# Kernel optimization log

Hardware: AMD Instinct MI355X
Metric: run time of the kernel (lower is better)

The kernel has to match this reference:

```python
import jax, jax.numpy as jnp
import numpy as np

HEADS = 16
HEAD_DIM = 64

def setup_inputs() -> dict:
    key = jax.random.key(0)
    ks = jax.random.split(key, 5)
    S, B, H = 1024, 4, 1024
    scale = 1.0 / np.sqrt(H)
    return {
        "hidden_states": jax.random.normal(ks[0], (S, B, H), jnp.float32),
        "attention_mask": jnp.zeros((B * HEADS, 1, S), jnp.float32),
        "Wq": jax.random.normal(ks[1], (H, H), jnp.float32) * scale,
        "bq": jnp.zeros((H,), jnp.float32),
        "Wk": jax.random.normal(ks[2], (H, H), jnp.float32) * scale,
        "bk": jnp.zeros((H,), jnp.float32),
        "Wv": jax.random.normal(ks[3], (H, H), jnp.float32) * scale,
        "bv": jnp.zeros((H,), jnp.float32),
    }

def reference(hidden_states, attention_mask, Wq, bq, Wk, bk, Wv, bv):
    S, B, H = hidden_states.shape
    d = HEAD_DIM
    inv_sqrt_d = 1.0 / np.sqrt(d)
    # QKV projections (torch Linear: x @ W.T + b)
    q = hidden_states @ Wq.T + bq  # (S, B, H)
    k = hidden_states @ Wk.T + bk
    v = hidden_states @ Wv.T + bv
    # (S, B*heads, d) -> (B*heads, S, d)
    q = q.reshape(S, B * HEADS, d).transpose(1, 0, 2)
    k = k.reshape(S, B * HEADS, d).transpose(1, 0, 2)
    v = v.reshape(S, B * HEADS, d).transpose(1, 0, 2)
    # SDDMM: scaled scores + additive mask -> (B*heads, S, S)
    scores = jnp.einsum('nsd,ntd->nst', q, k) * inv_sqrt_d + attention_mask
    probs = jax.nn.softmax(scores, axis=-1)
    # AV bmm -> (B*heads, S, d); note: dropout in source is seeded but never applied
    ctx = jnp.einsum('nst,ntd->nsd', probs, v)
    # back to (S, B, hidden)
    ctx = ctx.transpose(1, 0, 2).reshape(S, B, H)
    return ctx
```

## Files before the change

kernel.cpp:

```cpp
#include <hip/hip_runtime.h>
#include <hip/hip_bf16.h>
#include <math.h>

#define S_LEN 1024
#define BATCH 4
#define HID 1024
#define NHEADS 16
#define DHEAD 64
#define NTOT 64
#define M_ROWS 4096

typedef unsigned short u16;
typedef unsigned int u32;
typedef __bf16 bf16x8 __attribute__((ext_vector_type(8)));
typedef float f32x4 __attribute__((ext_vector_type(4)));

__device__ __forceinline__ u16 f2bf(float x) {
    __hip_bfloat16 h = __float2bfloat16(x);
    return *(u16*)&h;
}

__device__ __forceinline__ float fexp2(float x) {
#if __has_builtin(__builtin_amdgcn_exp2f)
    return __builtin_amdgcn_exp2f(x);
#else
    return __expf(x * 0.6931471805599453f);
#endif
}

__device__ __forceinline__ void gll16(const u16* g, u16* l) {
    __builtin_amdgcn_global_load_lds(
        (const __attribute__((address_space(1))) u32*)g,
        (__attribute__((address_space(3))) u32*)l, 16, 0, 0);
}

__global__ __launch_bounds__(256) void cvt_all(
    const float* __restrict__ X, const float* __restrict__ wq,
    const float* __restrict__ wk, const float* __restrict__ wv,
    u16* __restrict__ Xb, u16* __restrict__ Wb)
{
    const int bid = blockIdx.x;
    const float* src;
    u16* dst;
    size_t off;
    if (bid < 4096) {
        src = X; dst = Xb; off = (size_t)bid * 1024;
    } else {
        const int wb = bid - 4096;
        const int which = wb >> 10;
        src = (which == 0) ? wq : (which == 1) ? wk : wv;
        dst = Wb + (size_t)which * HID * HID;
        off = (size_t)(wb & 1023) * 1024;
    }
    const size_t idx = off + threadIdx.x * 4;
    float4 x = *(const float4*)(src + idx);
    *(ushort4*)(dst + idx) = make_ushort4(f2bf(x.x), f2bf(x.y), f2bf(x.z), f2bf(x.w));
}

__global__ __launch_bounds__(256, 3) void qkv_mfma(
    const u16* __restrict__ Xb, const u16* __restrict__ Wb,
    const float* __restrict__ bq, const float* __restrict__ bk,
    const float* __restrict__ bv,
    u16* __restrict__ Qb, u16* __restrict__ Kb, u16* __restrict__ VT)
{
    const int m0 = blockIdx.x * 128;
    const int n0 = blockIdx.y * 128;
    const int which = blockIdx.z;

    __shared__ __align__(16) u16 As[128 * 64];
    __shared__ __align__(16) u16 Bs[128 * 64];

    const int tid = threadIdx.x;
    const int lane = tid & 63;
    const int w = tid >> 6;
    const int wm = w & 1, wn = w >> 1;
    const int quad = lane >> 4;
    const int l15 = lane & 15;
    const int r7 = l15 & 7;

    const u16* W = Wb + (size_t)which * HID * HID;

    f32x4 acc[4][4];
    #pragma unroll
    for (int i = 0; i < 4; ++i)
        #pragma unroll
        for (int j = 0; j < 4; ++j)
            #pragma unroll
            for (int r = 0; r < 4; ++r) acc[i][j][r] = 0.0f;

    const int srow = lane >> 3;
    const int scg  = ((lane & 7) ^ srow) * 8;

    for (int k0 = 0; k0 < HID; k0 += 64) {
        #pragma unroll
        for (int c = 0; c < 4; ++c) {
            const int seg = w * 4 + c;
            const int row = seg * 8 + srow;
            gll16(Xb + (size_t)(m0 + row) * HID + k0 + scg, As + seg * 512);
            gll16(W  + (size_t)(n0 + row) * HID + k0 + scg, Bs + seg * 512);
        }
        __syncthreads();

        #pragma unroll
        for (int kk = 0; kk < 2; ++kk) {
            const int xo = ((kk * 4 + quad) ^ r7) * 8;
            bf16x8 af[4], bf[4];
            #pragma unroll
            for (int i = 0; i < 4; ++i)
                af[i] = *(const bf16x8*)(As + (wm * 64 + i * 16 + l15) * 64 + xo);
            #pragma unroll
            for (int j = 0; j < 4; ++j)
                bf[j] = *(const bf16x8*)(Bs + (wn * 64 + j * 16 + l15) * 64 + xo);
            #pragma unroll
            for (int i = 0; i < 4; ++i)
                #pragma unroll
                for (int j = 0; j < 4; ++j)
                    acc[i][j] = __builtin_amdgcn_mfma_f32_16x16x32_bf16(
                        af[i], bf[j], acc[i][j], 0, 0, 0);
        }
        __syncthreads();
    }

    const float* bias = (which == 0) ? bq : (which == 1) ? bk : bv;
    #pragma unroll
    for (int j = 0; j < 4; ++j) {
        const int o = n0 + wn * 64 + j * 16 + l15;
        const float bias_v = bias[o];
        const int head = o >> 6, d = o & 63;
        #pragma unroll
        for (int i = 0; i < 4; ++i) {
            const int mbase = m0 + wm * 64 + i * 16 + quad * 4;
            const int s = mbase >> 2;
            #pragma unroll
            for (int r = 0; r < 4; ++r) {
                const int n = r * NHEADS + head;
                const u16 hv = f2bf(acc[i][j][r] + bias_v);
                if (which == 0)
                    Qb[((size_t)n * S_LEN + s) * DHEAD + d] = hv;
                else if (which == 1)
                    Kb[((size_t)n * S_LEN + s) * DHEAD + d] = hv;
                else
                    VT[(size_t)n * (DHEAD * S_LEN) + (size_t)d * S_LEN + s] = hv;
            }
        }
    }
}

__global__ __launch_bounds__(256, 2) void attn_mfma(
    const u16* __restrict__ Qb, const u16* __restrict__ Kb,
    const u16* __restrict__ VT, const float* __restrict__ mask,
    float* __restrict__ out)
{
    const int bid = blockIdx.x;
    const int swz = (bid & 7) * 64 + (bid >> 3);
    const int n = swz >> 3;
    const int s0 = (swz & 7) * 128;
    const int b = n >> 4, head = n & 15;

    __shared__ __align__(16) char smem[51200];
    u16* Kbuf = (u16*)smem;
    u16* Vbuf = (u16*)(smem + 16384);
    u16* Ps   = (u16*)(smem + 32768);
    float* Of = (float*)smem;

    const int tid = threadIdx.x;
    const int lane = tid & 63;
    const int w = tid >> 6;
    const int quad = lane >> 4;
    const int l15 = lane & 15;
    const size_t nbase = (size_t)n * S_LEN * DHEAD;

    const int xs0 = ((quad ^ (l15 & 7)) * 8);
    const int xs1 = (((4 + quad) ^ (l15 & 7)) * 8);

    const int srow = lane >> 3;
    const int scg  = (lane & 7) ^ (srow & 7);

    bf16x8 qf[2][2];
    #pragma unroll
    for (int mi = 0; mi < 2; ++mi)
        #pragma unroll
        for (int st = 0; st < 2; ++st)
            qf[mi][st] = *(const bf16x8*)(Qb + nbase +
                (size_t)(s0 + w * 32 + mi * 16 + l15) * 64 + st * 32 + quad * 8);

    f32x4 O[2][4];
    float l_lane[2];
    #pragma unroll
    for (int mi = 0; mi < 2; ++mi) {
        l_lane[mi] = 0.0f;
        #pragma unroll
        for (int jt = 0; jt < 4; ++jt)
            #pragma unroll
            for (int r = 0; r < 4; ++r) O[mi][jt][r] = 0.0f;
    }

    {
        #pragma unroll
        for (int c = 0; c < 2; ++c) {
            const int seg = w * 2 + c;
            const int row = seg * 8 + srow;
            gll16(Kb + nbase + (size_t)row * 64 + scg * 8, Kbuf + seg * 512);
            gll16(VT + nbase + (size_t)row * S_LEN + scg * 8, Vbuf + seg * 512);
        }
    }
    __syncthreads();

    const float LOG2E = 1.44269504f;
    const float SCL2  = 0.18033688f;
    const float MOFF  = -23.0831099f;

    for (int it = 0; it < 16; ++it) {
        const int t0 = it * 64;
        const u16* kb = Kbuf + (it & 1) * 4096;
        const u16* vb = Vbuf + (it & 1) * 4096;

        if (it < 15) {
            u16* kd = Kbuf + ((it + 1) & 1) * 4096;
            u16* vd = Vbuf + ((it + 1) & 1) * 4096;
            #pragma unroll
            for (int c = 0; c < 2; ++c) {
                const int seg = w * 2 + c;
                const int row = seg * 8 + srow;
                gll16(Kb + nbase + (size_t)(t0 + 64 + row) * 64 + scg * 8, kd + seg * 512);
                gll16(VT + nbase + (size_t)row * S_LEN + t0 + 64 + scg * 8, vd + seg * 512);
            }
        }

        f32x4 sc[2][4];
        #pragma unroll
        for (int mi = 0; mi < 2; ++mi)
            #pragma unroll
            for (int j = 0; j < 4; ++j)
                #pragma unroll
                for (int r = 0; r < 4; ++r) sc[mi][j][r] = 0.0f;

        __builtin_amdgcn_s_setprio(1);
        #pragma unroll
        for (int st = 0; st < 2; ++st) {
            const int xo = st ? xs1 : xs0;
            bf16x8 kf[4];
            #pragma unroll
            for (int j = 0; j < 4; ++j)
                kf[j] = *(const bf16x8*)(kb + (j * 16 + l15) * 64 + xo);
            #pragma unroll
            for (int mi = 0; mi < 2; ++mi)
                #pragma unroll
                for (int j = 0; j < 4; ++j)
                    sc[mi][j] = __builtin_amdgcn_mfma_f32_16x16x32_bf16(
                        kf[j], qf[mi][st], sc[mi][j], 0, 0, 0);
        }
        __builtin_amdgcn_s_setprio(0);

        float4 mb4[4];
        #pragma unroll
        for (int j = 0; j < 4; ++j) {
            float4 mv = *(const float4*)(mask + (size_t)n * S_LEN + t0 + j * 16 + quad * 4);
            mb4[j].x = fmaf(mv.x, LOG2E, MOFF);
            mb4[j].y = fmaf(mv.y, LOG2E, MOFF);
            mb4[j].z = fmaf(mv.z, LOG2E, MOFF);
            mb4[j].w = fmaf(mv.w, LOG2E, MOFF);
        }

        #pragma unroll
        for (int mi = 0; mi < 2; ++mi) {
            const int q = w * 32 + mi * 16 + l15;
            #pragma unroll
            for (int j = 0; j < 4; ++j) {
                const float p0 = fexp2(fmaf(sc[mi][j][0], SCL2, mb4[j].x));
                const float p1 = fexp2(fmaf(sc[mi][j][1], SCL2, mb4[j].y));
                const float p2 = fexp2(fmaf(sc[mi][j][2], SCL2, mb4[j].z));
                const float p3 = fexp2(fmaf(sc[mi][j][3], SCL2, mb4[j].w));
                l_lane[mi] += (p0 + p1) + (p2 + p3);
                *(ushort4*)(Ps + q * 72 + j * 16 + quad * 4) =
                    make_ushort4(f2bf(p0), f2bf(p1), f2bf(p2), f2bf(p3));
            }
        }

        __builtin_amdgcn_s_setprio(1);
        #pragma unroll
        for (int st = 0; st < 2; ++st) {
            const int xo = st ? xs1 : xs0;
            bf16x8 vf[4];
            #pragma unroll
            for (int jt = 0; jt < 4; ++jt)
                vf[jt] = *(const bf16x8*)(vb + (jt * 16 + l15) * 64 + xo);
            #pragma unroll
            for (int mi = 0; mi < 2; ++mi) {
                bf16x8 pf = *(const bf16x8*)(Ps + (w * 32 + mi * 16 + l15) * 72 +
                                             st * 32 + quad * 8);
                #pragma unroll
                for (int jt = 0; jt < 4; ++jt)
                    O[mi][jt] = __builtin_amdgcn_mfma_f32_16x16x32_bf16(
                        vf[jt], pf, O[mi][jt], 0, 0, 0);
            }
        }
        __builtin_amdgcn_s_setprio(0);

        __syncthreads();
    }

    float inv_l[2];
    #pragma unroll
    for (int mi = 0; mi < 2; ++mi) {
        float l = l_lane[mi];
        l += __shfl_xor(l, 16);
        l += __shfl_xor(l, 32);
        inv_l[mi] = 1.0f / l;
    }
    __syncthreads();

    #pragma unroll
    for (int mi = 0; mi < 2; ++mi) {
        const int q = w * 32 + mi * 16 + l15;
        #pragma unroll
        for (int jt = 0; jt < 4; ++jt)
            #pragma unroll
            for (int r = 0; r < 4; ++r)
                Of[q * 72 + jt * 16 + quad * 4 + r] = O[mi][jt][r] * inv_l[mi];
    }
    __syncthreads();

    const int tx = tid & 15, ty = tid >> 4;
    #pragma unroll
    for (int p = 0; p < 8; ++p) {
        const int q = p * 16 + ty;
        float4 v = *(const float4*)(Of + q * 72 + tx * 4);
        *(float4*)(out + (size_t)(s0 + q) * (BATCH * HID) + (size_t)b * HID +
                   head * DHEAD + tx * 4) = v;
    }
}

extern "C" void kernel_launch(void* const* d_in, const int* in_sizes, int n_in,
                              void* d_out, int out_size, void* d_ws, size_t ws_size,
                              hipStream_t stream)
{
    const float* X    = (const float*)d_in[0];
    const float* mask = (const float*)d_in[1];
    const float* Wq   = (const float*)d_in[2];
    const float* bq   = (const float*)d_in[3];
    const float* Wk   = (const float*)d_in[4];
    const float* bk   = (const float*)d_in[5];
    const float* Wv   = (const float*)d_in[6];
    const float* bv   = (const float*)d_in[7];
    float* out = (float*)d_out;

    const size_t MX = (size_t)M_ROWS * HID;
    const size_t MW = (size_t)HID * HID;
    u16* wsp = (u16*)d_ws;
    u16* Xb = wsp;
    u16* Wb = Xb + MX;
    u16* Qb = Wb + 3 * MW;
    u16* Kb = Qb + MX;
    u16* VT = Kb + MX;

    cvt_all<<<dim3(4096 + 3072), 256, 0, stream>>>(X, Wq, Wk, Wv, Xb, Wb);
    qkv_mfma<<<dim3(M_ROWS / 128, HID / 128, 3), 256, 0, stream>>>(
        Xb, Wb, bq, bk, bv, Qb, Kb, VT);
    attn_mfma<<<dim3(S_LEN / 128 * NTOT), 256, 0, stream>>>(Qb, Kb, VT, mask, out);
}
```

Before: 149.2 us.

## Halve attention query tile to 64 rows and stage mask in LDS

Each attention block now handles 64 query rows instead of 128, with one 16-row MFMA tile per wave, so the grid doubles to 1024 blocks and launch bounds allow 3 blocks per CU. The mask row is loaded once into shared memory, already scaled and offset, rather than re-read from global memory every iteration. This aims to improve occupancy and load balance across CUs and to lower register pressure. In exchange each K/V tile is reused by half as many queries, so total K/V traffic from global memory and L2 doubles.

```diff
diff --git a/kernel.cpp b/kernel.cpp
--- a/kernel.cpp
+++ b/kernel.cpp
@@ -146,21 +146,22 @@
     }
 }
 
-__global__ __launch_bounds__(256, 2) void attn_mfma(
+__global__ __launch_bounds__(256, 3) void attn_mfma(
     const u16* __restrict__ Qb, const u16* __restrict__ Kb,
     const u16* __restrict__ VT, const float* __restrict__ mask,
     float* __restrict__ out)
 {
     const int bid = blockIdx.x;
-    const int swz = (bid & 7) * 64 + (bid >> 3);
-    const int n = swz >> 3;
-    const int s0 = (swz & 7) * 128;
+    const int swz = (bid & 7) * 128 + (bid >> 3);
+    const int n = swz >> 4;
+    const int s0 = (swz & 15) * 64;
     const int b = n >> 4, head = n & 15;
 
-    __shared__ __align__(16) char smem[51200];
+    __shared__ __align__(16) char smem[46080];
     u16* Kbuf = (u16*)smem;
     u16* Vbuf = (u16*)(smem + 16384);
     u16* Ps   = (u16*)(smem + 32768);
+    float* Ms = (float*)(smem + 41984);
     float* Of = (float*)smem;
 
     const int tid = threadIdx.x;
@@ -170,30 +171,37 @@
     const int l15 = lane & 15;
     const size_t nbase = (size_t)n * S_LEN * DHEAD;
 
+    const float LOG2E = 1.44269504f;
+    const float SCL2  = 0.18033688f;
+    const float MOFF  = -23.0831099f;
+
     const int xs0 = ((quad ^ (l15 & 7)) * 8);
     const int xs1 = (((4 + quad) ^ (l15 & 7)) * 8);
 
     const int srow = lane >> 3;
     const int scg  = (lane & 7) ^ (srow & 7);
 
-    bf16x8 qf[2][2];
-    #pragma unroll
-    for (int mi = 0; mi < 2; ++mi)
-        #pragma unroll
-        for (int st = 0; st < 2; ++st)
-            qf[mi][st] = *(const bf16x8*)(Qb + nbase +
-                (size_t)(s0 + w * 32 + mi * 16 + l15) * 64 + st * 32 + quad * 8);
-
-    f32x4 O[2][4];
-    float l_lane[2];
-    #pragma unroll
-    for (int mi = 0; mi < 2; ++mi) {
-        l_lane[mi] = 0.0f;
-        #pragma unroll
-        for (int jt = 0; jt < 4; ++jt)
-            #pragma unroll
-            for (int r = 0; r < 4; ++r) O[mi][jt][r] = 0.0f;
-    }
+    {
+        float4 mv = *(const float4*)(mask + (size_t)n * S_LEN + tid * 4);
+        Ms[tid * 4 + 0] = fmaf(mv.x, LOG2E, MOFF);
+        Ms[tid * 4 + 1] = fmaf(mv.y, LOG2E, MOFF);
+        Ms[tid * 4 + 2] = fmaf(mv.z, LOG2E, MOFF);
+        Ms[tid * 4 + 3] = fmaf(mv.w, LOG2E, MOFF);
+    }
+
+    const int q = w * 16 + l15;
+    bf16x8 qf[2];
+    #pragma unroll
+    for (int st = 0; st < 2; ++st)
+        qf[st] = *(const bf16x8*)(Qb + nbase +
+            (size_t)(s0 + q) * 64 + st * 32 + quad * 8);
+
+    f32x4 O[4];
+    float l_lane = 0.0f;
+    #pragma unroll
+    for (int jt = 0; jt < 4; ++jt)
+        #pragma unroll
+        for (int r = 0; r < 4; ++r) O[jt][r] = 0.0f;
 
     {
         #pragma unroll
@@ -205,10 +213,6 @@
         }
     }
     __syncthreads();
-
-    const float LOG2E = 1.44269504f;
-    const float SCL2  = 0.18033688f;
-    const float MOFF  = -23.0831099f;
 
     for (int it = 0; it < 16; ++it) {
         const int t0 = it * 64;
@@ -227,13 +231,11 @@
             }
         }
 
-        f32x4 sc[2][4];
-        #pragma unroll
-        for (int mi = 0; mi < 2; ++mi)
-            #pragma unroll
-            for (int j = 0; j < 4; ++j)
-                #pragma unroll
-                for (int r = 0; r < 4; ++r) sc[mi][j][r] = 0.0f;
+        f32x4 sc[4];
+        #pragma unroll
+        for (int j = 0; j < 4; ++j)
+            #pragma unroll
+            for (int r = 0; r < 4; ++r) sc[j][r] = 0.0f;
 
         __builtin_amdgcn_s_setprio(1);
         #pragma unroll
@@ -244,37 +246,22 @@
             for (int j = 0; j < 4; ++j)
                 kf[j] = *(const bf16x8*)(kb + (j * 16 + l15) * 64 + xo);
             #pragma unroll
-            for (int mi = 0; mi < 2; ++mi)
-                #pragma unroll
-                for (int j = 0; j < 4; ++j)
-                    sc[mi][j] = __builtin_amdgcn_mfma_f32_16x16x32_bf16(
-                        kf[j], qf[mi][st], sc[mi][j], 0, 0, 0);
+            for (int j = 0; j < 4; ++j)
+                sc[j] = __builtin_amdgcn_mfma_f32_16x16x32_bf16(
+                    kf[j], qf[st], sc[j], 0, 0, 0);
         }
         __builtin_amdgcn_s_setprio(0);
 
-        float4 mb4[4];
         #pragma unroll
         for (int j = 0; j < 4; ++j) {
-            float4 mv = *(const float4*)(mask + (size_t)n * S_LEN + t0 + j * 16 + quad * 4);
-            mb4[j].x = fmaf(mv.x, LOG2E, MOFF);
-            mb4[j].y = fmaf(mv.y, LOG2E, MOFF);
-            mb4[j].z = fmaf(mv.z, LOG2E, MOFF);
-            mb4[j].w = fmaf(mv.w, LOG2E, MOFF);
-        }
-
-        #pragma unroll
-        for (int mi = 0; mi < 2; ++mi) {
-            const int q = w * 32 + mi * 16 + l15;
-            #pragma unroll
-            for (int j = 0; j < 4; ++j) {
-                const float p0 = fexp2(fmaf(sc[mi][j][0], SCL2, mb4[j].x));
-                const float p1 = fexp2(fmaf(sc[mi][j][1], SCL2, mb4[j].y));
-                const float p2 = fexp2(fmaf(sc[mi][j][2], SCL2, mb4[j].z));
-                const float p3 = fexp2(fmaf(sc[mi][j][3], SCL2, mb4[j].w));
-                l_lane[mi] += (p0 + p1) + (p2 + p3);
-                *(ushort4*)(Ps + q * 72 + j * 16 + quad * 4) =
-                    make_ushort4(f2bf(p0), f2bf(p1), f2bf(p2), f2bf(p3));
-            }
+            float4 mb = *(const float4*)(Ms + t0 + j * 16 + quad * 4);
+            const float p0 = fexp2(fmaf(sc[j][0], SCL2, mb.x));
+            const float p1 = fexp2(fmaf(sc[j][1], SCL2, mb.y));
+            const float p2 = fexp2(fmaf(sc[j][2], SCL2, mb.z));
+            const float p3 = fexp2(fmaf(sc[j][3], SCL2, mb.w));
+            l_lane += (p0 + p1) + (p2 + p3);
+            *(ushort4*)(Ps + q * 72 + j * 16 + quad * 4) =
+                make_ushort4(f2bf(p0), f2bf(p1), f2bf(p2), f2bf(p3));
         }
 
         __builtin_amdgcn_s_setprio(1);
@@ -285,48 +272,36 @@
             #pragma unroll
             for (int jt = 0; jt < 4; ++jt)
                 vf[jt] = *(const bf16x8*)(vb + (jt * 16 + l15) * 64 + xo);
-            #pragma unroll
-            for (int mi = 0; mi < 2; ++mi) {
-                bf16x8 pf = *(const bf16x8*)(Ps + (w * 32 + mi * 16 + l15) * 72 +
-                                             st * 32 + quad * 8);
-                #pragma unroll
-                for (int jt = 0; jt < 4; ++jt)
-                    O[mi][jt] = __builtin_amdgcn_mfma_f32_16x16x32_bf16(
-                        vf[jt], pf, O[mi][jt], 0, 0, 0);
-            }
+            bf16x8 pf = *(const bf16x8*)(Ps + q * 72 + st * 32 + quad * 8);
+            #pragma unroll
+            for (int jt = 0; jt < 4; ++jt)
+                O[jt] = __builtin_amdgcn_mfma_f32_16x16x32_bf16(
+                    vf[jt], pf, O[jt], 0, 0, 0);
         }
         __builtin_amdgcn_s_setprio(0);
 
         __syncthreads();
     }
 
-    float inv_l[2];
-    #pragma unroll
-    for (int mi = 0; mi < 2; ++mi) {
-        float l = l_lane[mi];
-        l += __shfl_xor(l, 16);
-        l += __shfl_xor(l, 32);
-        inv_l[mi] = 1.0f / l;
-    }
+    float l = l_lane;
+    l += __shfl_xor(l, 16);
+    l += __shfl_xor(l, 32);
+    const float inv_l = 1.0f / l;
     __syncthreads();
 
     #pragma unroll
-    for (int mi = 0; mi < 2; ++mi) {
-        const int q = w * 32 + mi * 16 + l15;
-        #pragma unroll
-        for (int jt = 0; jt < 4; ++jt)
-            #pragma unroll
-            for (int r = 0; r < 4; ++r)
-                Of[q * 72 + jt * 16 + quad * 4 + r] = O[mi][jt][r] * inv_l[mi];
-    }
+    for (int jt = 0; jt < 4; ++jt)
+        #pragma unroll
+        for (int r = 0; r < 4; ++r)
+            Of[q * 72 + jt * 16 + quad * 4 + r] = O[jt][r] * inv_l;
     __syncthreads();
 
     const int tx = tid & 15, ty = tid >> 4;
     #pragma unroll
-    for (int p = 0; p < 8; ++p) {
-        const int q = p * 16 + ty;
-        float4 v = *(const float4*)(Of + q * 72 + tx * 4);
-        *(float4*)(out + (size_t)(s0 + q) * (BATCH * HID) + (size_t)b * HID +
+    for (int p = 0; p < 4; ++p) {
+        const int qq = p * 16 + ty;
+        float4 v = *(const float4*)(Of + qq * 72 + tx * 4);
+        *(float4*)(out + (size_t)(s0 + qq) * (BATCH * HID) + (size_t)b * HID +
                    head * DHEAD + tx * 4) = v;
     }
 }
@@ -357,5 +332,5 @@
     cvt_all<<<dim3(4096 + 3072), 256, 0, stream>>>(X, Wq, Wk, Wv, Xb, Wb);
     qkv_mfma<<<dim3(M_ROWS / 128, HID / 128, 3), 256, 0, stream>>>(
         Xb, Wb, bq, bk, bv, Qb, Kb, VT);
-    attn_mfma<<<dim3(S_LEN / 128 * NTOT), 256, 0, stream>>>(Qb, Kb, VT, mask, out);
-}
+    attn_mfma<<<dim3(S_LEN / 64 * NTOT), 256, 0, stream>>>(Qb, Kb, VT, mask, out);
+}
```

Measured after the change: 156.8 us. 1.05x slower.

## Keep softmax probabilities in registers via permlane swap instead of LDS round-trip

Applied to the files above, without the earlier changes.

The P matrix is no longer written to LDS and re-read as an MFMA operand. Probabilities are packed to bf16 with v_cvt_pk_bf16_f32 and rearranged across lanes with v_permlane16_swap, and the V fragment's k-index order is permuted to match. The mask row is also preloaded once into LDS, pre-scaled, instead of being read from global memory every iteration. LDS use drops, which could allow more occupancy, at the cost of inline asm and a more complex operand permutation that must be exactly right.

```diff
diff --git a/kernel.cpp b/kernel.cpp
--- a/kernel.cpp
+++ b/kernel.cpp
@@ -26,6 +26,16 @@
 #else
     return __expf(x * 0.6931471805599453f);
 #endif
+}
+
+__device__ __forceinline__ u32 cvtpk(float a, float b) {
+    u32 r;
+    asm("v_cvt_pk_bf16_f32 %0, %1, %2" : "=v"(r) : "v"(a), "v"(b));
+    return r;
+}
+
+__device__ __forceinline__ void pl16swap(u32& a, u32& b) {
+    asm("v_permlane16_swap_b32 %0, %1" : "+v"(a), "+v"(b));
 }
 
 __device__ __forceinline__ void gll16(const u16* g, u16* l) {
@@ -157,10 +167,10 @@
     const int s0 = (swz & 7) * 128;
     const int b = n >> 4, head = n & 15;
 
-    __shared__ __align__(16) char smem[51200];
+    __shared__ __align__(16) char smem[36864];
     u16* Kbuf = (u16*)smem;
     u16* Vbuf = (u16*)(smem + 16384);
-    u16* Ps   = (u16*)(smem + 32768);
+    float* Ms = (float*)(smem + 32768);
     float* Of = (float*)smem;
 
     const int tid = threadIdx.x;
@@ -168,13 +178,29 @@
     const int w = tid >> 6;
     const int quad = lane >> 4;
     const int l15 = lane & 15;
+    const int r7 = l15 & 7;
     const size_t nbase = (size_t)n * S_LEN * DHEAD;
 
-    const int xs0 = ((quad ^ (l15 & 7)) * 8);
-    const int xs1 = (((4 + quad) ^ (l15 & 7)) * 8);
+    const float LOG2E = 1.44269504f;
+    const float SCL2  = 0.18033688f;
+    const float MOFF  = -23.0831099f;
+
+    const int xs0 = ((quad ^ r7) * 8);
+    const int xs1 = (((4 + quad) ^ r7) * 8);
+    const int qperm = ((quad & 1) << 1) | (quad >> 1);
+    const int xv0 = ((qperm ^ r7) * 8);
+    const int xv1 = (((4 + qperm) ^ r7) * 8);
 
     const int srow = lane >> 3;
     const int scg  = (lane & 7) ^ (srow & 7);
+
+    {
+        float4 mv = *(const float4*)(mask + (size_t)n * S_LEN + tid * 4);
+        Ms[tid * 4 + 0] = fmaf(mv.x, LOG2E, MOFF);
+        Ms[tid * 4 + 1] = fmaf(mv.y, LOG2E, MOFF);
+        Ms[tid * 4 + 2] = fmaf(mv.z, LOG2E, MOFF);
+        Ms[tid * 4 + 3] = fmaf(mv.w, LOG2E, MOFF);
+    }
 
     bf16x8 qf[2][2];
     #pragma unroll
@@ -205,10 +231,6 @@
         }
     }
     __syncthreads();
-
-    const float LOG2E = 1.44269504f;
-    const float SCL2  = 0.18033688f;
-    const float MOFF  = -23.0831099f;
 
     for (int it = 0; it < 16; ++it) {
         const int t0 = it * 64;
@@ -254,45 +276,50 @@
 
         float4 mb4[4];
         #pragma unroll
-        for (int j = 0; j < 4; ++j) {
-            float4 mv = *(const float4*)(mask + (size_t)n * S_LEN + t0 + j * 16 + quad * 4);
-            mb4[j].x = fmaf(mv.x, LOG2E, MOFF);
-            mb4[j].y = fmaf(mv.y, LOG2E, MOFF);
-            mb4[j].z = fmaf(mv.z, LOG2E, MOFF);
-            mb4[j].w = fmaf(mv.w, LOG2E, MOFF);
-        }
-
+        for (int j = 0; j < 4; ++j)
+            mb4[j] = *(const float4*)(Ms + t0 + j * 16 + quad * 4);
+
+        u32 pw[2][2][4];
         #pragma unroll
         for (int mi = 0; mi < 2; ++mi) {
-            const int q = w * 32 + mi * 16 + l15;
+            float pj[4][4];
             #pragma unroll
             for (int j = 0; j < 4; ++j) {
-                const float p0 = fexp2(fmaf(sc[mi][j][0], SCL2, mb4[j].x));
-                const float p1 = fexp2(fmaf(sc[mi][j][1], SCL2, mb4[j].y));
-                const float p2 = fexp2(fmaf(sc[mi][j][2], SCL2, mb4[j].z));
-                const float p3 = fexp2(fmaf(sc[mi][j][3], SCL2, mb4[j].w));
-                l_lane[mi] += (p0 + p1) + (p2 + p3);
-                *(ushort4*)(Ps + q * 72 + j * 16 + quad * 4) =
-                    make_ushort4(f2bf(p0), f2bf(p1), f2bf(p2), f2bf(p3));
+                pj[j][0] = fexp2(fmaf(sc[mi][j][0], SCL2, mb4[j].x));
+                pj[j][1] = fexp2(fmaf(sc[mi][j][1], SCL2, mb4[j].y));
+                pj[j][2] = fexp2(fmaf(sc[mi][j][2], SCL2, mb4[j].z));
+                pj[j][3] = fexp2(fmaf(sc[mi][j][3], SCL2, mb4[j].w));
+                l_lane[mi] += (pj[j][0] + pj[j][1]) + (pj[j][2] + pj[j][3]);
             }
+            u32 W00 = cvtpk(pj[0][0], pj[0][1]), W01 = cvtpk(pj[0][2], pj[0][3]);
+            u32 W10 = cvtpk(pj[1][0], pj[1][1]), W11 = cvtpk(pj[1][2], pj[1][3]);
+            u32 W20 = cvtpk(pj[2][0], pj[2][1]), W21 = cvtpk(pj[2][2], pj[2][3]);
+            u32 W30 = cvtpk(pj[3][0], pj[3][1]), W31 = cvtpk(pj[3][2], pj[3][3]);
+            pl16swap(W00, W10); pl16swap(W01, W11);
+            pl16swap(W20, W30); pl16swap(W21, W31);
+            pw[mi][0][0] = W00; pw[mi][0][1] = W01;
+            pw[mi][0][2] = W10; pw[mi][0][3] = W11;
+            pw[mi][1][0] = W20; pw[mi][1][1] = W21;
+            pw[mi][1][2] = W30; pw[mi][1][3] = W31;
         }
 
         __builtin_amdgcn_s_setprio(1);
         #pragma unroll
         for (int st = 0; st < 2; ++st) {
-            const int xo = st ? xs1 : xs0;
+            const int xo = st ? xv1 : xv0;
             bf16x8 vf[4];
             #pragma unroll
             for (int jt = 0; jt < 4; ++jt)
                 vf[jt] = *(const bf16x8*)(vb + (jt * 16 + l15) * 64 + xo);
             #pragma unroll
             for (int mi = 0; mi < 2; ++mi) {
-                bf16x8 pf = *(const bf16x8*)(Ps + (w * 32 + mi * 16 + l15) * 72 +
-                                             st * 32 + quad * 8);
+                union { u32 wds[4]; bf16x8 v; } pu;
+                pu.wds[0] = pw[mi][st][0]; pu.wds[1] = pw[mi][st][1];
+                pu.wds[2] = pw[mi][st][2]; pu.wds[3] = pw[mi][st][3];
                 #pragma unroll
                 for (int jt = 0; jt < 4; ++jt)
                     O[mi][jt] = __builtin_amdgcn_mfma_f32_16x16x32_bf16(
-                        vf[jt], pf, O[mi][jt], 0, 0, 0);
+                        vf[jt], pu.v, O[mi][jt], 0, 0, 0);
             }
         }
         __builtin_amdgcn_s_setprio(0);
```

Measured after the change: 146.5 us. About the same (-1.8%).
